# Optimization experiments

Measured on AMD Instinct MI355X. Metric: run time of the kernel, lower is better.

The kernel has to match this reference:

```python
import jax, jax.numpy as jnp
import numpy as np

B, S, HID = 1, 2048, 1024
H, HKV, D = 16, 4, 64
THETA = 10000.0


def _rope_tables(seq_len, head_dim):
    # Matches RotaryEmbedding: emb = cat(freqs, freqs); kernel reads cos/sin at even
    # positions d for each rotated pair (d, d+1), i.e. columns 0::2 of the table.
    inv_freq = 1.0 / (THETA ** (jnp.arange(0, head_dim, 2, dtype=jnp.float32) / head_dim))
    freqs = jnp.arange(seq_len, dtype=jnp.float32)[:, None] * inv_freq[None, :]  # [S, D/2]
    emb = jnp.concatenate([freqs, freqs], axis=-1)  # [S, D]
    return jnp.cos(emb)[:, 0::2], jnp.sin(emb)[:, 0::2]  # each [S, D/2]


def _apply_rope(x, cos, sin):
    # x: [B, H, S, D]; rotate interleaved pairs (2i, 2i+1) as in the kernel.
    xe, xo = x[..., 0::2], x[..., 1::2]
    re = xe * cos - xo * sin
    ro = xe * sin + xo * cos
    return jnp.stack([re, ro], axis=-1).reshape(x.shape)


def setup_inputs() -> dict:
    key = jax.random.key(0)
    k0, k1, k2, k3, k4 = jax.random.split(key, 5)
    return {
        "hidden_states": jax.random.normal(k0, (B, S, HID), dtype=jnp.float32),
        "Wq": jax.random.normal(k1, (HID, H * D), dtype=jnp.float32) * 0.02,
        "Wk": jax.random.normal(k2, (HID, HKV * D), dtype=jnp.float32) * 0.02,
        "Wv": jax.random.normal(k3, (HID, HKV * D), dtype=jnp.float32) * 0.02,
        "Wo": jax.random.normal(k4, (H * D, HID), dtype=jnp.float32) * 0.02,
    }


def reference(hidden_states, Wq, Wk, Wv, Wo):
    b, s, _ = hidden_states.shape
    q = (hidden_states @ Wq).reshape(b, s, H, D).transpose(0, 2, 1, 3)    # [B,H,S,D]
    k = (hidden_states @ Wk).reshape(b, s, HKV, D).transpose(0, 2, 1, 3)  # [B,Hkv,S,D]
    v = (hidden_states @ Wv).reshape(b, s, HKV, D).transpose(0, 2, 1, 3)

    cos, sin = _rope_tables(s, D)
    q = _apply_rope(q, cos, sin)
    k = _apply_rope(k, cos, sin)

    G = H // HKV  # GQA group size: query head h -> kv head h // G
    qg = q.reshape(b, HKV, G, s, D)
    scale = jnp.float32(D) ** -0.5
    scores = jnp.einsum("bkgqd,bkpd->bkgqp", qg, k) * scale  # [B,Hkv,G,S,S]
    causal = jnp.tril(jnp.ones((s, s), dtype=bool))
    scores = jnp.where(causal, scores, jnp.float32(-1e30))
    probs = jax.nn.softmax(scores, axis=-1)
    out = jnp.einsum("bkgqp,bkpd->bkgqd", probs, v).reshape(b, H, s, D)
    out = out.transpose(0, 2, 1, 3).reshape(b, s, H * D)
    return out @ Wo
```

## Files before the change

### kernel.cpp

```cpp
#include <hip/hip_runtime.h>
#include <hip/hip_bf16.h>
#include <math.h>

#define SEQ   2048
#define HID   1024
#define NH    16
#define NKV   4
#define DH    64
#define GQ    (NH / NKV)
#define NQKV  1536
#define LQKV  1536
#define KT    64
#define QB    32
#define CH    512
#define NCH   (SEQ / CH)
#define PSTR  72

typedef __attribute__((ext_vector_type(8))) short bf16x8;
typedef __attribute__((ext_vector_type(4))) float f32x4;
typedef unsigned short u16;
typedef unsigned int u32;

__device__ __forceinline__ u16 f2bf(float f) {
    union { float f; unsigned u; } x; x.f = f;
    unsigned r = x.u + 0x7fffu + ((x.u >> 16) & 1u);
    return (u16)(r >> 16);
}
__device__ __forceinline__ u32 pk2bf(float lo, float hi) {
    return (u32)f2bf(lo) | ((u32)f2bf(hi) << 16);
}
__device__ __forceinline__ void load_lds16(const u16* g, u16* l) {
    __builtin_amdgcn_global_load_lds(
        (const __attribute__((address_space(1))) unsigned int*)g,
        (__attribute__((address_space(3))) unsigned int*)l, 16, 0, 0);
}

__global__ __launch_bounds__(256) void setup(const float* __restrict__ X,
                                             const float* __restrict__ Wq,
                                             const float* __restrict__ Wk,
                                             const float* __restrict__ Wv,
                                             const float* __restrict__ Wo,
                                             u16* __restrict__ Xb,
                                             u16* __restrict__ Wt,
                                             u16* __restrict__ WoT) {
    const int z = blockIdx.z;
    if (z == 4) {
        const int idx = ((int)blockIdx.y * 64 + (int)blockIdx.x) * 256 + threadIdx.x;
        const float4 v = ((const float4*)X)[idx];
        ushort4 o;
        o.x = f2bf(v.x); o.y = f2bf(v.y); o.z = f2bf(v.z); o.w = f2bf(v.w);
        ((ushort4*)Xb)[idx] = o;
        return;
    }
    const float* in; u16* out; int N;
    if (z == 0)      { in = Wq; out = Wt;                             N = HID; }
    else if (z == 1) { in = Wk; out = Wt + (size_t)HID * HID;         N = 256; }
    else if (z == 2) { in = Wv; out = Wt + (size_t)(HID + 256) * HID; N = 256; }
    else             { in = Wo; out = WoT;                            N = HID; }

    const int n0 = blockIdx.x * 32;
    if (n0 >= N) return;
    const int k0 = blockIdx.y * 32;

    __shared__ float t[32][33];
    const int tx = threadIdx.x & 31;
    const int ty = threadIdx.x >> 5;
    #pragma unroll
    for (int i = 0; i < 4; ++i)
        t[ty + i * 8][tx] = in[(size_t)(k0 + ty + i * 8) * N + n0 + tx];
    __syncthreads();
    #pragma unroll
    for (int i = 0; i < 4; ++i)
        out[(size_t)(n0 + ty + i * 8) * HID + k0 + tx] = f2bf(t[tx][ty + i * 8]);
}

__global__ __launch_bounds__(256) void gemm_v2(const u16* __restrict__ A,
                                               const u16* __restrict__ Bt,
                                               float* __restrict__ C,
                                               int K, int ldc) {
    __shared__ u16 Bs[2][64 * 32];

    const int tid  = threadIdx.x;
    const int lane = tid & 63;
    const int w    = tid >> 6;
    const int c    = lane & 15;
    const int quad = lane >> 4;
    const int m0   = blockIdx.y * 128;
    const int n0   = blockIdx.x * 64;

    const u16* gB  = Bt + (size_t)(n0 + w * 16 + (lane >> 2)) * K + (lane & 3) * 8;
    u16* const bdst = (u16*)&Bs[0][0] + (w * 16) * 32;

    const u16* gA0 = A + (size_t)(m0 + w * 32 + c) * K + quad * 8;
    const u16* gA1 = gA0 + (size_t)16 * K;

    const int T = K / 32;

    f32x4 acc[2][4];
    #pragma unroll
    for (int mt = 0; mt < 2; ++mt)
        #pragma unroll
        for (int nt = 0; nt < 4; ++nt)
            acc[mt][nt] = (f32x4){0.f, 0.f, 0.f, 0.f};

    bf16x8 afc[2], afn[2];
    afc[0] = *(const bf16x8*)gA0;
    afc[1] = *(const bf16x8*)gA1;
    load_lds16(gB, bdst);

    for (int t = 0; t < T; ++t) {
        __syncthreads();
        if (t + 1 < T) {
            load_lds16(gB + (t + 1) * 32, bdst + ((t + 1) & 1) * (64 * 32));
            afn[0] = *(const bf16x8*)(gA0 + (t + 1) * 32);
            afn[1] = *(const bf16x8*)(gA1 + (t + 1) * 32);
        }
        bf16x8 bfr[4];
        #pragma unroll
        for (int nt = 0; nt < 4; ++nt)
            bfr[nt] = *(const bf16x8*)&Bs[t & 1][(nt * 16 + c) * 32 + quad * 8];
        #pragma unroll
        for (int mt = 0; mt < 2; ++mt)
            #pragma unroll
            for (int nt = 0; nt < 4; ++nt)
                acc[mt][nt] = __builtin_amdgcn_mfma_f32_16x16x32_bf16(afc[mt], bfr[nt], acc[mt][nt], 0, 0, 0);
        afc[0] = afn[0];
        afc[1] = afn[1];
    }

    #pragma unroll
    for (int mt = 0; mt < 2; ++mt)
        #pragma unroll
        for (int nt = 0; nt < 4; ++nt)
            #pragma unroll
            for (int rg = 0; rg < 4; ++rg)
                C[(size_t)(m0 + w * 32 + mt * 16 + quad * 4 + rg) * ldc + n0 + nt * 16 + c] = acc[mt][nt][rg];
}

__global__ __launch_bounds__(256) void postprocess(const float* __restrict__ QKV,
                                                   u16* __restrict__ Qb,
                                                   u16* __restrict__ Kb,
                                                   u16* __restrict__ VTg) {
    const int s   = blockIdx.x;
    const int tid = threadIdx.x;
    const float* row = QKV + (size_t)s * LQKV;
    const float ln_scale = 9.210340371976184f / 32.0f;

    #pragma unroll
    for (int it = 0; it < 2; ++it) {
        const int p = tid + it * 256;
        const int j = p & 31;
        const float inv_freq = __expf(-(float)((2 * j) & 31) * ln_scale);
        float sn, cs;
        __sincosf((float)s * inv_freq, &sn, &cs);
        const float xe = row[2 * p], xo = row[2 * p + 1];
        Qb[(size_t)s * HID + 2 * p]     = f2bf((xe * cs - xo * sn) * 0.125f);
        Qb[(size_t)s * HID + 2 * p + 1] = f2bf((xe * sn + xo * cs) * 0.125f);
    }
    if (tid < 128) {
        const int p  = tid;
        const int j  = p & 31;
        const int kh = p >> 5;
        const int d  = (2 * p) & 63;
        const float inv_freq = __expf(-(float)((2 * j) & 31) * ln_scale);
        float sn, cs;
        __sincosf((float)s * inv_freq, &sn, &cs);
        const float xe = row[1024 + 2 * p], xo = row[1024 + 2 * p + 1];
        u16* kr = Kb + ((size_t)kh * SEQ + s) * DH;
        kr[d]     = f2bf(xe * cs - xo * sn);
        kr[d + 1] = f2bf(xe * sn + xo * cs);
    }
    {
        const int c = tid;
        const int kh = c >> 6, d = c & 63;
        VTg[((size_t)kh * DH + d) * SEQ + s] = f2bf(row[1280 + c]);
    }
}

__global__ __launch_bounds__(256) void attn_kernel(const u16* __restrict__ Qb,
                                                   const u16* __restrict__ Kb,
                                                   const u16* __restrict__ VTg,
                                                   float* __restrict__ Opart,
                                                   float* __restrict__ lpart) {
    __shared__ u16 Kst[64 * PSTR];
    __shared__ u16 VTst[64 * PSTR];
    __shared__ u16 Pst[4][QB * PSTR];

    const int tid  = threadIdx.x;
    const int lane = tid & 63;
    const int w    = tid >> 6;
    const int c    = lane & 15;
    const int quad = lane >> 4;
    const int kh   = blockIdx.y;
    const int z    = blockIdx.z;
    const int qt   = (SEQ / QB - 1) - (int)blockIdx.x;
    const int q0   = qt * QB;
    const int h    = kh * GQ + w;

    const int kstart = z * CH;
    const int klim   = q0 + QB;
    if (kstart >= klim) return;
    const int kend   = (klim < kstart + CH) ? klim : (kstart + CH);
    const int ntiles = (kend - kstart + KT - 1) / KT;

    bf16x8 qf[2][2];
    #pragma unroll
    for (int g = 0; g < 2; ++g)
        #pragma unroll
        for (int ks = 0; ks < 2; ++ks)
            qf[g][ks] = *(const bf16x8*)&Qb[(size_t)(q0 + g * 16 + c) * HID + h * DH + ks * 32 + quad * 8];

    f32x4 accO[4][2];
    #pragma unroll
    for (int nt = 0; nt < 4; ++nt)
        #pragma unroll
        for (int g = 0; g < 2; ++g)
            accO[nt][g] = (f32x4){0.f, 0.f, 0.f, 0.f};
    float l[2] = {0.f, 0.f};

    for (int t = 0; t < ntiles; ++t) {
        const int kt0 = kstart + t * KT;
        __syncthreads();
        {
            const int r = tid >> 3, off = (tid & 7) * 8;
            const u16* kg = &Kb[((size_t)kh * SEQ + kt0 + r) * DH + off];
            *(uint4*)&Kst[r * PSTR + off]        = *(const uint4*)kg;
            *(uint4*)&Kst[(r + 32) * PSTR + off] = *(const uint4*)(kg + 32 * DH);
            const u16* vg = &VTg[((size_t)kh * DH + r) * SEQ + kt0 + off];
            *(uint4*)&VTst[r * PSTR + off]        = *(const uint4*)vg;
            *(uint4*)&VTst[(r + 32) * PSTR + off] = *(const uint4*)(vg + 32 * SEQ);
        }
        __syncthreads();

        f32x4 accS[4][2];
        #pragma unroll
        for (int nS = 0; nS < 4; ++nS)
            #pragma unroll
            for (int g = 0; g < 2; ++g)
                accS[nS][g] = (f32x4){0.f, 0.f, 0.f, 0.f};
        #pragma unroll
        for (int nS = 0; nS < 4; ++nS)
            #pragma unroll
            for (int ks = 0; ks < 2; ++ks) {
                const bf16x8 kf = *(const bf16x8*)&Kst[(nS * 16 + c) * PSTR + ks * 32 + quad * 8];
                #pragma unroll
                for (int g = 0; g < 2; ++g)
                    accS[nS][g] = __builtin_amdgcn_mfma_f32_16x16x32_bf16(kf, qf[g][ks], accS[nS][g], 0, 0, 0);
            }

        #pragma unroll
        for (int g = 0; g < 2; ++g) {
            const int q = q0 + g * 16 + c;
            #pragma unroll
            for (int nS = 0; nS < 4; ++nS) {
                const int key = kt0 + nS * 16 + quad * 4;
                const float p0 = (key + 0 <= q) ? __expf(accS[nS][g][0]) : 0.f;
                const float p1 = (key + 1 <= q) ? __expf(accS[nS][g][1]) : 0.f;
                const float p2 = (key + 2 <= q) ? __expf(accS[nS][g][2]) : 0.f;
                const float p3 = (key + 3 <= q) ? __expf(accS[nS][g][3]) : 0.f;
                l[g] += (p0 + p1) + (p2 + p3);
                u32* dst = (u32*)&Pst[w][(g * 16 + c) * PSTR + nS * 16 + quad * 4];
                dst[0] = pk2bf(p0, p1);
                dst[1] = pk2bf(p2, p3);
            }
        }
        __threadfence_block();

        #pragma unroll
        for (int ks2 = 0; ks2 < 2; ++ks2) {
            bf16x8 pf[2];
            #pragma unroll
            for (int g = 0; g < 2; ++g)
                pf[g] = *(const bf16x8*)&Pst[w][(g * 16 + c) * PSTR + ks2 * 32 + quad * 8];
            #pragma unroll
            for (int nt = 0; nt < 4; ++nt) {
                const bf16x8 vf = *(const bf16x8*)&VTst[(nt * 16 + c) * PSTR + ks2 * 32 + quad * 8];
                #pragma unroll
                for (int g = 0; g < 2; ++g)
                    accO[nt][g] = __builtin_amdgcn_mfma_f32_16x16x32_bf16(vf, pf[g], accO[nt][g], 0, 0, 0);
            }
        }
    }

    #pragma unroll
    for (int g = 0; g < 2; ++g) {
        float lg = l[g];
        lg += __shfl_xor(lg, 16);
        lg += __shfl_xor(lg, 32);
        if (quad == 0)
            lpart[((size_t)z * SEQ + q0 + g * 16 + c) * NH + h] = lg;

        float* Op = Opart + ((size_t)z * SEQ + q0 + g * 16 + c) * HID + h * DH;
        #pragma unroll
        for (int nt = 0; nt < 4; ++nt)
            *(f32x4*)&Op[nt * 16 + quad * 4] = accO[nt][g];
    }
}

__global__ __launch_bounds__(256) void attn_reduce(const float* __restrict__ Opart,
                                                   const float* __restrict__ lpart,
                                                   u16* __restrict__ At) {
    const int idx = blockIdx.x * 256 + threadIdx.x;
    const int q  = idx >> 8;
    const int h  = (idx & 255) >> 4;
    const int klim = (q & ~(QB - 1)) + QB;
    float4 o = ((const float4*)Opart)[idx];
    float  l = lpart[q * NH + h];
    #pragma unroll
    for (int z = 1; z < NCH; ++z) {
        if (z * CH < klim) {
            const float4 o1 = ((const float4*)Opart)[idx + z * (SEQ * HID / 4)];
            o.x += o1.x; o.y += o1.y; o.z += o1.z; o.w += o1.w;
            l += lpart[(z * SEQ + q) * NH + h];
        }
    }
    const float inv = 1.0f / l;
    ushort4 r;
    r.x = f2bf(o.x * inv); r.y = f2bf(o.y * inv);
    r.z = f2bf(o.z * inv); r.w = f2bf(o.w * inv);
    ((ushort4*)At)[idx] = r;
}

extern "C" void kernel_launch(void* const* d_in, const int* in_sizes, int n_in,
                              void* d_out, int out_size, void* d_ws, size_t ws_size,
                              hipStream_t stream) {
    const float* X  = (const float*)d_in[0];
    const float* Wq = (const float*)d_in[1];
    const float* Wk = (const float*)d_in[2];
    const float* Wv = (const float*)d_in[3];
    const float* Wo = (const float*)d_in[4];
    float* out = (float*)d_out;

    u16* Wt     = (u16*)d_ws;
    u16* WoT    = Wt + (size_t)NQKV * HID;
    u16* Xb     = WoT + (size_t)HID * HID;
    u16* At     = Xb + (size_t)SEQ * HID;
    u16* Qb     = At + (size_t)SEQ * HID;
    u16* Kb     = Qb + (size_t)SEQ * HID;
    u16* VTg    = Kb + (size_t)NKV * SEQ * DH;
    float* QKVc = (float*)(VTg + (size_t)NKV * DH * SEQ);
    float* Opart = QKVc;
    float* lpart = Opart + (size_t)NCH * SEQ * HID;

    dim3 blk(256);

    setup<<<dim3(64, 32, 5), blk, 0, stream>>>(X, Wq, Wk, Wv, Wo, Xb, Wt, WoT);

    gemm_v2<<<dim3(NQKV / 64, SEQ / 128), blk, 0, stream>>>(Xb, Wt, QKVc, HID, LQKV);

    postprocess<<<SEQ, blk, 0, stream>>>(QKVc, Qb, Kb, VTg);

    attn_kernel<<<dim3(SEQ / QB, NKV, NCH), blk, 0, stream>>>(Qb, Kb, VTg, Opart, lpart);

    attn_reduce<<<(SEQ * HID / 4) / 256, blk, 0, stream>>>(Opart, lpart, At);

    gemm_v2<<<dim3(HID / 64, SEQ / 128), blk, 0, stream>>>(At, WoT, out, HID, HID);
}
```

Measured before the change: 158.6 us.

## Load K/V fragments directly from global with register prefetch, drop LDS staging

The attention kernel no longer stages K and V^T tiles in shared memory behind block-wide barriers. Each wave loads its MFMA fragments straight from global memory and prefetches the next K tile into registers. Query tiles shrink from 32 to 16 rows and key tiles from 64 to 32, which doubles the grid and removes both __syncthreads per tile. In exchange, the four waves of a block (which share a KV head) each fetch the same K/V data separately, adding global and L2 traffic and giving less reuse per load.

Measured after the change: 212.7 us. +34.1%, slower.

```diff
diff --git a/kernel.cpp b/kernel.cpp
--- a/kernel.cpp
+++ b/kernel.cpp
@@ -10,11 +10,10 @@
 #define GQ    (NH / NKV)
 #define NQKV  1536
 #define LQKV  1536
-#define KT    64
-#define QB    32
+#define KT    32
 #define CH    512
 #define NCH   (SEQ / CH)
-#define PSTR  72
+#define PPS   40
 
 typedef __attribute__((ext_vector_type(8))) short bf16x8;
 typedef __attribute__((ext_vector_type(4))) float f32x4;
@@ -182,9 +181,7 @@
                                                    const u16* __restrict__ VTg,
                                                    float* __restrict__ Opart,
                                                    float* __restrict__ lpart) {
-    __shared__ u16 Kst[64 * PSTR];
-    __shared__ u16 VTst[64 * PSTR];
-    __shared__ u16 Pst[4][QB * PSTR];
+    __shared__ u16 Pst[4][16 * PPS];
 
     const int tid  = threadIdx.x;
     const int lane = tid & 63;
@@ -193,108 +190,97 @@
     const int quad = lane >> 4;
     const int kh   = blockIdx.y;
     const int z    = blockIdx.z;
-    const int qt   = (SEQ / QB - 1) - (int)blockIdx.x;
-    const int q0   = qt * QB;
+    const int qt   = (SEQ / 16 - 1) - (int)blockIdx.x;
+    const int q0   = qt * 16;
     const int h    = kh * GQ + w;
 
     const int kstart = z * CH;
-    const int klim   = q0 + QB;
+    const int klim   = q0 + 16;
     if (kstart >= klim) return;
     const int kend   = (klim < kstart + CH) ? klim : (kstart + CH);
     const int ntiles = (kend - kstart + KT - 1) / KT;
 
-    bf16x8 qf[2][2];
-    #pragma unroll
-    for (int g = 0; g < 2; ++g)
+    bf16x8 qf[2];
+    #pragma unroll
+    for (int ks = 0; ks < 2; ++ks)
+        qf[ks] = *(const bf16x8*)&Qb[(size_t)(q0 + c) * HID + h * DH + ks * 32 + quad * 8];
+
+    const u16* Kfrag = Kb  + ((size_t)kh * SEQ + kstart + c) * DH + quad * 8;
+    const u16* Vfrag = VTg + ((size_t)kh * DH + c) * SEQ + kstart + quad * 8;
+
+    f32x4 accO[4];
+    #pragma unroll
+    for (int nt = 0; nt < 4; ++nt) accO[nt] = (f32x4){0.f, 0.f, 0.f, 0.f};
+    float l = 0.f;
+
+    bf16x8 kf[2][2], kn[2][2];
+    #pragma unroll
+    for (int nS = 0; nS < 2; ++nS)
         #pragma unroll
         for (int ks = 0; ks < 2; ++ks)
-            qf[g][ks] = *(const bf16x8*)&Qb[(size_t)(q0 + g * 16 + c) * HID + h * DH + ks * 32 + quad * 8];
-
-    f32x4 accO[4][2];
-    #pragma unroll
-    for (int nt = 0; nt < 4; ++nt)
-        #pragma unroll
-        for (int g = 0; g < 2; ++g)
-            accO[nt][g] = (f32x4){0.f, 0.f, 0.f, 0.f};
-    float l[2] = {0.f, 0.f};
+            kf[nS][ks] = *(const bf16x8*)(Kfrag + (size_t)(nS * 16) * DH + ks * 32);
 
     for (int t = 0; t < ntiles; ++t) {
-        const int kt0 = kstart + t * KT;
-        __syncthreads();
-        {
-            const int r = tid >> 3, off = (tid & 7) * 8;
-            const u16* kg = &Kb[((size_t)kh * SEQ + kt0 + r) * DH + off];
-            *(uint4*)&Kst[r * PSTR + off]        = *(const uint4*)kg;
-            *(uint4*)&Kst[(r + 32) * PSTR + off] = *(const uint4*)(kg + 32 * DH);
-            const u16* vg = &VTg[((size_t)kh * DH + r) * SEQ + kt0 + off];
-            *(uint4*)&VTst[r * PSTR + off]        = *(const uint4*)vg;
-            *(uint4*)&VTst[(r + 32) * PSTR + off] = *(const uint4*)(vg + 32 * SEQ);
+        const int kt0 = t * KT;
+
+        bf16x8 vf[4];
+        #pragma unroll
+        for (int nt = 0; nt < 4; ++nt)
+            vf[nt] = *(const bf16x8*)(Vfrag + (size_t)(nt * 16) * SEQ + kt0);
+
+        f32x4 accS[2];
+        #pragma unroll
+        for (int nS = 0; nS < 2; ++nS) accS[nS] = (f32x4){0.f, 0.f, 0.f, 0.f};
+        #pragma unroll
+        for (int nS = 0; nS < 2; ++nS)
+            #pragma unroll
+            for (int ks = 0; ks < 2; ++ks)
+                accS[nS] = __builtin_amdgcn_mfma_f32_16x16x32_bf16(kf[nS][ks], qf[ks], accS[nS], 0, 0, 0);
+
+        if (t + 1 < ntiles) {
+            #pragma unroll
+            for (int nS = 0; nS < 2; ++nS)
+                #pragma unroll
+                for (int ks = 0; ks < 2; ++ks)
+                    kn[nS][ks] = *(const bf16x8*)(Kfrag + (size_t)(kt0 + KT + nS * 16) * DH + ks * 32);
         }
-        __syncthreads();
-
-        f32x4 accS[4][2];
-        #pragma unroll
-        for (int nS = 0; nS < 4; ++nS)
-            #pragma unroll
-            for (int g = 0; g < 2; ++g)
-                accS[nS][g] = (f32x4){0.f, 0.f, 0.f, 0.f};
-        #pragma unroll
-        for (int nS = 0; nS < 4; ++nS)
-            #pragma unroll
-            for (int ks = 0; ks < 2; ++ks) {
-                const bf16x8 kf = *(const bf16x8*)&Kst[(nS * 16 + c) * PSTR + ks * 32 + quad * 8];
-                #pragma unroll
-                for (int g = 0; g < 2; ++g)
-                    accS[nS][g] = __builtin_amdgcn_mfma_f32_16x16x32_bf16(kf, qf[g][ks], accS[nS][g], 0, 0, 0);
-            }
-
-        #pragma unroll
-        for (int g = 0; g < 2; ++g) {
-            const int q = q0 + g * 16 + c;
-            #pragma unroll
-            for (int nS = 0; nS < 4; ++nS) {
-                const int key = kt0 + nS * 16 + quad * 4;
-                const float p0 = (key + 0 <= q) ? __expf(accS[nS][g][0]) : 0.f;
-                const float p1 = (key + 1 <= q) ? __expf(accS[nS][g][1]) : 0.f;
-                const float p2 = (key + 2 <= q) ? __expf(accS[nS][g][2]) : 0.f;
-                const float p3 = (key + 3 <= q) ? __expf(accS[nS][g][3]) : 0.f;
-                l[g] += (p0 + p1) + (p2 + p3);
-                u32* dst = (u32*)&Pst[w][(g * 16 + c) * PSTR + nS * 16 + quad * 4];
-                dst[0] = pk2bf(p0, p1);
-                dst[1] = pk2bf(p2, p3);
-            }
+
+        const int q = q0 + c;
+        #pragma unroll
+        for (int nS = 0; nS < 2; ++nS) {
+            const int key = kstart + kt0 + nS * 16 + quad * 4;
+            const float p0 = (key + 0 <= q) ? __expf(accS[nS][0]) : 0.f;
+            const float p1 = (key + 1 <= q) ? __expf(accS[nS][1]) : 0.f;
+            const float p2 = (key + 2 <= q) ? __expf(accS[nS][2]) : 0.f;
+            const float p3 = (key + 3 <= q) ? __expf(accS[nS][3]) : 0.f;
+            l += (p0 + p1) + (p2 + p3);
+            u32* dst = (u32*)&Pst[w][c * PPS + nS * 16 + quad * 4];
+            dst[0] = pk2bf(p0, p1);
+            dst[1] = pk2bf(p2, p3);
         }
         __threadfence_block();
 
-        #pragma unroll
-        for (int ks2 = 0; ks2 < 2; ++ks2) {
-            bf16x8 pf[2];
-            #pragma unroll
-            for (int g = 0; g < 2; ++g)
-                pf[g] = *(const bf16x8*)&Pst[w][(g * 16 + c) * PSTR + ks2 * 32 + quad * 8];
-            #pragma unroll
-            for (int nt = 0; nt < 4; ++nt) {
-                const bf16x8 vf = *(const bf16x8*)&VTst[(nt * 16 + c) * PSTR + ks2 * 32 + quad * 8];
-                #pragma unroll
-                for (int g = 0; g < 2; ++g)
-                    accO[nt][g] = __builtin_amdgcn_mfma_f32_16x16x32_bf16(vf, pf[g], accO[nt][g], 0, 0, 0);
-            }
-        }
-    }
-
-    #pragma unroll
-    for (int g = 0; g < 2; ++g) {
-        float lg = l[g];
-        lg += __shfl_xor(lg, 16);
-        lg += __shfl_xor(lg, 32);
-        if (quad == 0)
-            lpart[((size_t)z * SEQ + q0 + g * 16 + c) * NH + h] = lg;
-
-        float* Op = Opart + ((size_t)z * SEQ + q0 + g * 16 + c) * HID + h * DH;
-        #pragma unroll
-        for (int nt = 0; nt < 4; ++nt)
-            *(f32x4*)&Op[nt * 16 + quad * 4] = accO[nt][g];
-    }
+        const bf16x8 pf = *(const bf16x8*)&Pst[w][c * PPS + quad * 8];
+        #pragma unroll
+        for (int nt = 0; nt < 4; ++nt)
+            accO[nt] = __builtin_amdgcn_mfma_f32_16x16x32_bf16(vf[nt], pf, accO[nt], 0, 0, 0);
+
+        #pragma unroll
+        for (int nS = 0; nS < 2; ++nS)
+            #pragma unroll
+            for (int ks = 0; ks < 2; ++ks)
+                kf[nS][ks] = kn[nS][ks];
+    }
+
+    l += __shfl_xor(l, 16);
+    l += __shfl_xor(l, 32);
+    if (quad == 0)
+        lpart[((size_t)z * SEQ + q0 + c) * NH + h] = l;
+
+    float* Op = Opart + ((size_t)z * SEQ + q0 + c) * HID + h * DH;
+    #pragma unroll
+    for (int nt = 0; nt < 4; ++nt)
+        *(f32x4*)&Op[nt * 16 + quad * 4] = accO[nt];
 }
 
 __global__ __launch_bounds__(256) void attn_reduce(const float* __restrict__ Opart,
@@ -303,7 +289,7 @@
     const int idx = blockIdx.x * 256 + threadIdx.x;
     const int q  = idx >> 8;
     const int h  = (idx & 255) >> 4;
-    const int klim = (q & ~(QB - 1)) + QB;
+    const int klim = (q & ~15) + 16;
     float4 o = ((const float4*)Opart)[idx];
     float  l = lpart[q * NH + h];
     #pragma unroll
@@ -350,7 +336,7 @@
 
     postprocess<<<SEQ, blk, 0, stream>>>(QKVc, Qb, Kb, VTg);
 
-    attn_kernel<<<dim3(SEQ / QB, NKV, NCH), blk, 0, stream>>>(Qb, Kb, VTg, Opart, lpart);
+    attn_kernel<<<dim3(SEQ / 16, NKV, NCH), blk, 0, stream>>>(Qb, Kb, VTg, Opart, lpart);
 
     attn_reduce<<<(SEQ * HID / 4) / 256, blk, 0, stream>>>(Opart, lpart, At);
 
```
